# Kernel tuning notes

Hardware: AMD Instinct MI355X
Metric: run time of the kernel (lower is better)

Reference implementation:

```python
import jax, jax.numpy as jnp
import numpy as np

NC = 16       # class_nums
C = 128       # in_channel == EMBEND_DIM
NS = 8192     # support points
NQ = 30000    # query points
EPS = 1e-8


def setup_inputs() -> dict:
    key = jax.random.key(0)
    ks = jax.random.split(key, 7)
    support_features = jax.random.normal(ks[0], (NS, C), dtype=jnp.float32)
    support_labels = jax.random.randint(ks[1], (NS,), 0, NC)
    query_features = jax.random.normal(ks[2], (NQ, C), dtype=jnp.float32)
    # proj = Linear(2C+1 -> C) + ReLU + Linear(C -> 128)
    s1 = 1.0 / np.sqrt(2 * C + 1)
    W1 = jax.random.uniform(ks[3], (2 * C + 1, C), minval=-s1, maxval=s1, dtype=jnp.float32)
    b1 = jax.random.uniform(ks[4], (C,), minval=-s1, maxval=s1, dtype=jnp.float32)
    s2 = 1.0 / np.sqrt(C)
    W2 = jax.random.uniform(ks[5], (C, C), minval=-s2, maxval=s2, dtype=jnp.float32)
    b2 = jax.random.uniform(ks[6], (C,), minval=-s2, maxval=s2, dtype=jnp.float32)
    return {"support_features": support_features, "support_labels": support_labels,
            "query_features": query_features, "W1": W1, "b1": b1, "W2": W2, "b2": b2}


def _prototypes(support_features, support_labels):
    # fused scatter-mean replacing the per-class Python loop
    sums = jax.ops.segment_sum(support_features, support_labels, num_segments=NC)  # [Nc, C]
    counts = jax.ops.segment_sum(jnp.ones((support_features.shape[0],), support_features.dtype),
                                 support_labels, num_segments=NC)                   # [Nc]
    return jnp.where(counts[:, None] > 0, sums / jnp.maximum(counts, 1.0)[:, None], 0.0)


def reference(support_features, support_labels, query_features, W1, b1, W2, b2):
    protos = _prototypes(support_features, support_labels)                # [Nc, C]
    # MD_distance: cosine similarity between each query and each class prototype
    qn = query_features / jnp.maximum(jnp.linalg.norm(query_features, axis=-1, keepdims=True), EPS)
    pn = protos / jnp.maximum(jnp.linalg.norm(protos, axis=-1, keepdims=True), EPS)
    cos = jnp.einsum('qc,nc->qn', qn, pn)                                 # [Nq, Nc]
    # proj(cat([query, proto, cos], -1)) without materializing the [Nq,Nc,2C+1] concat:
    # split W1 rows into query part, proto part, and cos part.
    Wq, Wp, Wc = W1[:C], W1[C:2 * C], W1[2 * C]                           # [C,C],[C,C],[C]
    h = jax.nn.relu(jnp.einsum('qc,ch->qh', query_features, Wq)[:, None, :]
                    + jnp.einsum('nc,ch->nh', protos, Wp)[None, :, :]
                    + cos[:, :, None] * Wc[None, None, :]
                    + b1)                                                 # [Nq, Nc, C]
    similarity = jnp.einsum('qnh,ho->qno', h, W2) + b2                    # [Nq, Nc, 128]
    return similarity, cos[:, :, None]
```

## Files before the change

kernel.cpp:

```cpp
#include <hip/hip_runtime.h>

#define NQ_ 30000
#define NC_ 16
#define C_  128
#define NS_ 8192
#define QB  16
#define NBLK (NQ_/QB)

typedef __attribute__((ext_vector_type(4))) float  f32x4;
typedef __attribute__((ext_vector_type(8))) short  s16x8;

#define WS_PART  0
#define WS_PCNT  65536
#define WS_T     66048
#define WS_PACK  68096

__device__ inline short f2bf(float x){
  unsigned u = __float_as_uint(x);
  u += 0x7fffu + ((u >> 16) & 1u);
  return (short)(u >> 16);
}

__global__ __launch_bounds__(256) void protoA(const float* __restrict__ sf,
                                              const int* __restrict__ lbl,
                                              const float* __restrict__ W1,
                                              const float* __restrict__ W2,
                                              float* __restrict__ ws){
  const int b = blockIdx.x;
  const int t = threadIdx.x;
  if (b < 256){
    __shared__ int ll[512];
    const int cls = b >> 4;
    const int ch  = b & 15;
    const int r0  = ch * 512;
    *(int2*)&ll[t*2] = *(const int2*)&lbl[r0 + t*2];
    __syncthreads();
    const int sub = t >> 7;
    const int c   = t & 127;
    const int i0  = sub * 256;
    float s0 = 0.f, s1 = 0.f; int cnt = 0;
    #pragma unroll 4
    for (int i = 0; i < 256; i += 2){
      if (ll[i0+i]   == cls){ s0 += sf[(size_t)(r0+i0+i  )*C_ + c]; ++cnt; }
      if (ll[i0+i+1] == cls){ s1 += sf[(size_t)(r0+i0+i+1)*C_ + c]; ++cnt; }
    }
    ws[WS_PART + ((size_t)(cls*32 + ch*2 + sub))*C_ + c] = s0 + s1;
    if (c == 0) ws[WS_PCNT + cls*32 + ch*2 + sub] = (float)cnt;
  } else {
    short* packo = (short*)(ws + WS_PACK);
    const int g0 = (b - 256)*2048 + t*8;
    const int gg = g0 & 16383;
    const int ln = (gg >> 3) & 63, ks = (gg >> 9) & 3, wvv = gg >> 11;
    const int kb = ks*32 + ((ln >> 4) & 3)*8;
    const int col = wvv*16 + (ln & 15);
    const float* src = (g0 < 16384) ? W2 : W1;
    s16x8 v;
    #pragma unroll
    for (int i = 0; i < 8; ++i) v[i] = f2bf(src[(size_t)(kb + i)*C_ + col]);
    *(s16x8*)&packo[g0] = v;
  }
}

__global__ __launch_bounds__(128) void protoB(const float* __restrict__ W1,
                                              const float* __restrict__ b1,
                                              float* __restrict__ ws){
  __shared__ float pr[C_];
  __shared__ float rns;
  const int n = blockIdx.x;
  const int h = threadIdx.x;
  float s = 0.f;
  #pragma unroll 8
  for (int ch = 0; ch < 32; ++ch) s += ws[WS_PART + ((size_t)(n*32 + ch))*C_ + h];
  float cnt = 0.f;
  #pragma unroll 8
  for (int ch = 0; ch < 32; ++ch) cnt += ws[WS_PCNT + n*32 + ch];
  const float pv = (cnt > 0.f) ? s / fmaxf(cnt, 1.f) : 0.f;
  pr[h] = pv;
  __syncthreads();
  if (h < 64){
    float q = pr[h]*pr[h] + pr[h+64]*pr[h+64];
    q += __shfl_xor(q, 1);  q += __shfl_xor(q, 2);  q += __shfl_xor(q, 4);
    q += __shfl_xor(q, 8);  q += __shfl_xor(q, 16); q += __shfl_xor(q, 32);
    if (h == 0) rns = 1.f / fmaxf(sqrtf(q), 1e-8f);
  }
  __syncthreads();
  {
    short* packo = (short*)(ws + WS_PACK);
    const int k = h;
    const int gg = ((k >> 5)*64 + ((k >> 3) & 3)*16 + n)*8 + (k & 7);
    packo[32768 + gg] = f2bf(pv * rns);
  }
  float acc = b1[h];
  #pragma unroll 8
  for (int c = 0; c < C_; ++c) acc = fmaf(pr[c], W1[(size_t)(C_ + c)*C_ + h], acc);
  ws[WS_T + n*C_ + h] = acc;
}

__global__ __launch_bounds__(256, 4) void fused_main(const float* __restrict__ qfeat,
                                                     const float* __restrict__ W1,
                                                     const float* __restrict__ b2,
                                                     const float* __restrict__ ws,
                                                     float* __restrict__ out){
  __shared__ __align__(16) char un[16384];
  __shared__ float qw[QB][132];
  __shared__ float tl16[NC_][132];
  __shared__ float cosl[QB][NC_];
  __shared__ float rqn[QB];
  __shared__ float wcl[C_];

  float (*qfs)[132] = (float(*)[132])un;
  short* hfrag = (short*)un;

  const int t    = threadIdx.x;
  const int lane = t & 63;
  const int wv   = t >> 6;
  const int fr   = lane & 15;
  const int fg   = lane >> 4;
  const int qbase = blockIdx.x * QB;
  float* out_cos = out + (size_t)NQ_ * NC_ * C_;
  const short* pack = (const short*)(ws + WS_PACK);

  {
    const int idx = t * 8, q = idx >> 7, c = idx & 127;
    *(f32x4*)&qfs[q][c]      = *(const f32x4*)(qfeat + (size_t)qbase*C_ + idx);
    *(f32x4*)&qfs[q][c+4]    = *(const f32x4*)(qfeat + (size_t)qbase*C_ + idx + 4);
    *(f32x4*)&tl16[q][c]     = *(const f32x4*)(ws + WS_T + idx);
    *(f32x4*)&tl16[q][c+4]   = *(const f32x4*)(ws + WS_T + idx + 4);
    if (t < 32) *(f32x4*)&wcl[t*4] = *(const f32x4*)(W1 + 2*C_*C_ + t*4);
  }
  __syncthreads();

  if (t < 128){
    int q = t >> 3; int c0 = (t & 7) * 16;
    float s = 0.f;
    #pragma unroll
    for (int m = 0; m < 16; ++m){ float v = qfs[q][c0+m]; s = fmaf(v, v, s); }
    s += __shfl_xor(s, 1); s += __shfl_xor(s, 2); s += __shfl_xor(s, 4);
    if ((t & 7) == 0) rqn[q] = 1.f / fmaxf(sqrtf(s), 1e-8f);
  }

  s16x8 qfr[4];
  #pragma unroll
  for (int ks = 0; ks < 4; ++ks){
    const int c0 = ks*32 + fg*8;
    f32x4 a = *(const f32x4*)&qfs[fr][c0];
    f32x4 b = *(const f32x4*)&qfs[fr][c0+4];
    s16x8 v;
    v[0]=f2bf(a[0]); v[1]=f2bf(a[1]); v[2]=f2bf(a[2]); v[3]=f2bf(a[3]);
    v[4]=f2bf(b[0]); v[5]=f2bf(b[1]); v[6]=f2bf(b[2]); v[7]=f2bf(b[3]);
    qfr[ks] = v;
  }
  s16x8 w2f[2][4];
  float b2v[2];
  #pragma unroll
  for (int j = 0; j < 2; ++j){
    const int tt = wv*2 + j;
    #pragma unroll
    for (int ks = 0; ks < 4; ++ks)
      w2f[j][ks] = *(const s16x8*)&pack[((tt*4 + ks)*64 + lane)*8];
    b2v[j] = b2[tt*16 + fr];
  }
  __syncthreads();

  #pragma unroll
  for (int j = 0; j < 2; ++j){
    const int tt = wv*2 + j;
    f32x4 dq = {0.f,0.f,0.f,0.f};
    #pragma unroll
    for (int ks = 0; ks < 4; ++ks)
      dq = __builtin_amdgcn_mfma_f32_16x16x32_bf16(qfr[ks],
             *(const s16x8*)&pack[16384 + ((tt*4 + ks)*64 + lane)*8], dq, 0,0,0);
    #pragma unroll
    for (int r = 0; r < 4; ++r) qw[fg*4 + r][tt*16 + fr] = dq[r];
  }
  if (wv == 0){
    f32x4 dc = {0.f,0.f,0.f,0.f};
    #pragma unroll
    for (int ks = 0; ks < 4; ++ks)
      dc = __builtin_amdgcn_mfma_f32_16x16x32_bf16(qfr[ks],
             *(const s16x8*)&pack[32768 + (ks*64 + lane)*8], dc, 0,0,0);
    #pragma unroll
    for (int r = 0; r < 4; ++r){
      const int q = fg*4 + r;
      const float cv = dc[r] * rqn[q];
      cosl[q][fr] = cv;
      out_cos[(size_t)(qbase + q)*NC_ + fr] = cv;
    }
  }
  __syncthreads();

  const int k0 = wv*32 + fg*8;
  const f32x4 t8a = *(const f32x4*)&tl16[fr][k0];
  const f32x4 t8b = *(const f32x4*)&tl16[fr][k0+4];
  const f32x4 w8a = *(const f32x4*)&wcl[k0];
  const f32x4 w8b = *(const f32x4*)&wcl[k0+4];

  #pragma unroll
  for (int chunk = 0; chunk < 4; ++chunk){
    const int q0 = chunk * 4;
    #pragma unroll
    for (int qq = 0; qq < 4; ++qq){
      const int q = q0 + qq;
      f32x4 qa = *(const f32x4*)&qw[q][k0];
      f32x4 qb = *(const f32x4*)&qw[q][k0+4];
      const float cv = cosl[q][fr];
      s16x8 hv;
      #pragma unroll
      for (int jj = 0; jj < 4; ++jj)
        hv[jj] = f2bf(fmaxf(fmaf(cv, w8a[jj], qa[jj] + t8a[jj]), 0.f));
      #pragma unroll
      for (int jj = 0; jj < 4; ++jj)
        hv[4+jj] = f2bf(fmaxf(fmaf(cv, w8b[jj], qb[jj] + t8b[jj]), 0.f));
      *(s16x8*)&hfrag[qq*2048 + wv*512 + lane*8] = hv;
    }
    __syncthreads();
    #pragma unroll
    for (int qq = 0; qq < 4; ++qq){
      const short* hb = &hfrag[qq*2048 + lane*8];
      s16x8 a0 = *(const s16x8*)&hb[0];
      s16x8 a1 = *(const s16x8*)&hb[512];
      s16x8 a2 = *(const s16x8*)&hb[1024];
      s16x8 a3 = *(const s16x8*)&hb[1536];
      const size_t qout = (size_t)(qbase + q0 + qq) * (NC_*C_);
      #pragma unroll
      for (int j = 0; j < 2; ++j){
        f32x4 acc = {b2v[j], b2v[j], b2v[j], b2v[j]};
        acc = __builtin_amdgcn_mfma_f32_16x16x32_bf16(a0, w2f[j][0], acc, 0,0,0);
        acc = __builtin_amdgcn_mfma_f32_16x16x32_bf16(a1, w2f[j][1], acc, 0,0,0);
        acc = __builtin_amdgcn_mfma_f32_16x16x32_bf16(a2, w2f[j][2], acc, 0,0,0);
        acc = __builtin_amdgcn_mfma_f32_16x16x32_bf16(a3, w2f[j][3], acc, 0,0,0);
        const int ocol = (wv*2 + j)*16 + fr;
        #pragma unroll
        for (int r = 0; r < 4; ++r)
          out[qout + (fg*4 + r)*C_ + ocol] = acc[r];
      }
    }
    __syncthreads();
  }
}

extern "C" void kernel_launch(void* const* d_in, const int* in_sizes, int n_in,
                              void* d_out, int out_size, void* d_ws, size_t ws_size,
                              hipStream_t stream){
  const float* sf  = (const float*)d_in[0];
  const int*   lbl = (const int*)  d_in[1];
  const float* qf  = (const float*)d_in[2];
  const float* W1  = (const float*)d_in[3];
  const float* b1  = (const float*)d_in[4];
  const float* W2  = (const float*)d_in[5];
  const float* b2  = (const float*)d_in[6];
  float* ws  = (float*)d_ws;
  float* out = (float*)d_out;

  protoA<<<272, 256, 0, stream>>>(sf, lbl, W1, W2, ws);
  protoB<<<NC_, 128, 0, stream>>>(W1, b1, ws);
  fused_main<<<NBLK, 256, 0, stream>>>(qf, W1, b2, ws, out);
}
```

Baseline: 82.12 us.

## Process 32 queries per block in fused kernel and split protoB matvec across 512 threads

The fused main kernel now handles 32 queries per block instead of 16. It computes two sets of query MFMA fragments, and two waves compute the cosine tile, so the per-block setup (tl16, W2 fragments, wc, syncs) is amortized over twice as many queries. Bounds checks were added because 30000 is not a multiple of 32. protoB splits the 128-long prototype×W1 matvec across four thread groups, with a shared-memory reduction to shorten its serial chain. The trade-offs are fewer blocks and lower occupancy (launch bounds drop from 4 to 3 blocks) plus more registers per thread.

```diff
diff --git a/kernel.cpp b/kernel.cpp
--- a/kernel.cpp
+++ b/kernel.cpp
@@ -4,8 +4,8 @@
 #define NC_ 16
 #define C_  128
 #define NS_ 8192
-#define QB  16
-#define NBLK (NQ_/QB)
+#define QB2 32
+#define NBLK2 ((NQ_ + QB2 - 1)/QB2)
 
 typedef __attribute__((ext_vector_type(4))) float  f32x4;
 typedef __attribute__((ext_vector_type(8))) short  s16x8;
@@ -61,51 +61,57 @@
   }
 }
 
-__global__ __launch_bounds__(128) void protoB(const float* __restrict__ W1,
+__global__ __launch_bounds__(512) void protoB(const float* __restrict__ W1,
                                               const float* __restrict__ b1,
                                               float* __restrict__ ws){
   __shared__ float pr[C_];
+  __shared__ float sacc[4][C_];
   __shared__ float rns;
   const int n = blockIdx.x;
-  const int h = threadIdx.x;
-  float s = 0.f;
-  #pragma unroll 8
-  for (int ch = 0; ch < 32; ++ch) s += ws[WS_PART + ((size_t)(n*32 + ch))*C_ + h];
-  float cnt = 0.f;
-  #pragma unroll 8
-  for (int ch = 0; ch < 32; ++ch) cnt += ws[WS_PCNT + n*32 + ch];
-  const float pv = (cnt > 0.f) ? s / fmaxf(cnt, 1.f) : 0.f;
-  pr[h] = pv;
-  __syncthreads();
-  if (h < 64){
-    float q = pr[h]*pr[h] + pr[h+64]*pr[h+64];
+  const int t = threadIdx.x;
+  const int h = t & 127;
+  const int part = t >> 7;
+  if (t < 128){
+    float s = 0.f, cnt = 0.f;
+    #pragma unroll 8
+    for (int ch = 0; ch < 32; ++ch) s   += ws[WS_PART + ((size_t)(n*32 + ch))*C_ + h];
+    #pragma unroll 8
+    for (int ch = 0; ch < 32; ++ch) cnt += ws[WS_PCNT + n*32 + ch];
+    pr[h] = (cnt > 0.f) ? s / fmaxf(cnt, 1.f) : 0.f;
+  }
+  __syncthreads();
+  if (t < 64){
+    float q = pr[t]*pr[t] + pr[t+64]*pr[t+64];
     q += __shfl_xor(q, 1);  q += __shfl_xor(q, 2);  q += __shfl_xor(q, 4);
     q += __shfl_xor(q, 8);  q += __shfl_xor(q, 16); q += __shfl_xor(q, 32);
-    if (h == 0) rns = 1.f / fmaxf(sqrtf(q), 1e-8f);
-  }
-  __syncthreads();
+    if (t == 0) rns = 1.f / fmaxf(sqrtf(q), 1e-8f);
+  }
   {
+    float a = 0.f;
+    const int c0 = part * 32;
+    #pragma unroll 8
+    for (int c = c0; c < c0 + 32; ++c) a = fmaf(pr[c], W1[(size_t)(C_ + c)*C_ + h], a);
+    sacc[part][h] = a;
+  }
+  __syncthreads();
+  if (t < 128){
     short* packo = (short*)(ws + WS_PACK);
-    const int k = h;
-    const int gg = ((k >> 5)*64 + ((k >> 3) & 3)*16 + n)*8 + (k & 7);
-    packo[32768 + gg] = f2bf(pv * rns);
-  }
-  float acc = b1[h];
-  #pragma unroll 8
-  for (int c = 0; c < C_; ++c) acc = fmaf(pr[c], W1[(size_t)(C_ + c)*C_ + h], acc);
-  ws[WS_T + n*C_ + h] = acc;
-}
-
-__global__ __launch_bounds__(256, 4) void fused_main(const float* __restrict__ qfeat,
+    const int gg = ((h >> 5)*64 + ((h >> 3) & 3)*16 + n)*8 + (h & 7);
+    packo[32768 + gg] = f2bf(pr[h] * rns);
+    ws[WS_T + n*C_ + h] = b1[h] + ((sacc[0][h] + sacc[1][h]) + (sacc[2][h] + sacc[3][h]));
+  }
+}
+
+__global__ __launch_bounds__(256, 3) void fused_main(const float* __restrict__ qfeat,
                                                      const float* __restrict__ W1,
                                                      const float* __restrict__ b2,
                                                      const float* __restrict__ ws,
                                                      float* __restrict__ out){
-  __shared__ __align__(16) char un[16384];
-  __shared__ float qw[QB][132];
+  __shared__ __align__(16) char un[16896];
+  __shared__ float qw[QB2][132];
   __shared__ float tl16[NC_][132];
-  __shared__ float cosl[QB][NC_];
-  __shared__ float rqn[QB];
+  __shared__ float cosl[QB2][NC_];
+  __shared__ float rqn[QB2];
   __shared__ float wcl[C_];
 
   float (*qfs)[132] = (float(*)[132])un;
@@ -116,22 +122,27 @@
   const int wv   = t >> 6;
   const int fr   = lane & 15;
   const int fg   = lane >> 4;
-  const int qbase = blockIdx.x * QB;
+  const int qbase = blockIdx.x * QB2;
   float* out_cos = out + (size_t)NQ_ * NC_ * C_;
   const short* pack = (const short*)(ws + WS_PACK);
 
   {
-    const int idx = t * 8, q = idx >> 7, c = idx & 127;
-    *(f32x4*)&qfs[q][c]      = *(const f32x4*)(qfeat + (size_t)qbase*C_ + idx);
-    *(f32x4*)&qfs[q][c+4]    = *(const f32x4*)(qfeat + (size_t)qbase*C_ + idx + 4);
-    *(f32x4*)&tl16[q][c]     = *(const f32x4*)(ws + WS_T + idx);
-    *(f32x4*)&tl16[q][c+4]   = *(const f32x4*)(ws + WS_T + idx + 4);
+    const int q = t >> 3, c = (t & 7) * 16;
+    int gr = qbase + q; if (gr > NQ_ - 1) gr = NQ_ - 1;
+    const float* src = qfeat + (size_t)gr*C_ + c;
+    *(f32x4*)&qfs[q][c]    = *(const f32x4*)(src);
+    *(f32x4*)&qfs[q][c+4]  = *(const f32x4*)(src + 4);
+    *(f32x4*)&qfs[q][c+8]  = *(const f32x4*)(src + 8);
+    *(f32x4*)&qfs[q][c+12] = *(const f32x4*)(src + 12);
+    const int r2 = t >> 4, c2 = (t & 15) * 8;
+    *(f32x4*)&tl16[r2][c2]   = *(const f32x4*)(ws + WS_T + r2*C_ + c2);
+    *(f32x4*)&tl16[r2][c2+4] = *(const f32x4*)(ws + WS_T + r2*C_ + c2 + 4);
     if (t < 32) *(f32x4*)&wcl[t*4] = *(const f32x4*)(W1 + 2*C_*C_ + t*4);
   }
   __syncthreads();
 
-  if (t < 128){
-    int q = t >> 3; int c0 = (t & 7) * 16;
+  {
+    const int q = t >> 3, c0 = (t & 7) * 16;
     float s = 0.f;
     #pragma unroll
     for (int m = 0; m < 16; ++m){ float v = qfs[q][c0+m]; s = fmaf(v, v, s); }
@@ -139,7 +150,7 @@
     if ((t & 7) == 0) rqn[q] = 1.f / fmaxf(sqrtf(s), 1e-8f);
   }
 
-  s16x8 qfr[4];
+  s16x8 qfrA[4], qfrB[4];
   #pragma unroll
   for (int ks = 0; ks < 4; ++ks){
     const int c0 = ks*32 + fg*8;
@@ -148,7 +159,13 @@
     s16x8 v;
     v[0]=f2bf(a[0]); v[1]=f2bf(a[1]); v[2]=f2bf(a[2]); v[3]=f2bf(a[3]);
     v[4]=f2bf(b[0]); v[5]=f2bf(b[1]); v[6]=f2bf(b[2]); v[7]=f2bf(b[3]);
-    qfr[ks] = v;
+    qfrA[ks] = v;
+    f32x4 a2 = *(const f32x4*)&qfs[fr+16][c0];
+    f32x4 b2x = *(const f32x4*)&qfs[fr+16][c0+4];
+    s16x8 w;
+    w[0]=f2bf(a2[0]); w[1]=f2bf(a2[1]); w[2]=f2bf(a2[2]); w[3]=f2bf(a2[3]);
+    w[4]=f2bf(b2x[0]); w[5]=f2bf(b2x[1]); w[6]=f2bf(b2x[2]); w[7]=f2bf(b2x[3]);
+    qfrB[ks] = w;
   }
   s16x8 w2f[2][4];
   float b2v[2];
@@ -163,28 +180,32 @@
   __syncthreads();
 
   #pragma unroll
-  for (int j = 0; j < 2; ++j){
-    const int tt = wv*2 + j;
-    f32x4 dq = {0.f,0.f,0.f,0.f};
+  for (int g = 0; g < 2; ++g){
+    #pragma unroll
+    for (int j = 0; j < 2; ++j){
+      const int tt = wv*2 + j;
+      f32x4 dq = {0.f,0.f,0.f,0.f};
+      #pragma unroll
+      for (int ks = 0; ks < 4; ++ks)
+        dq = __builtin_amdgcn_mfma_f32_16x16x32_bf16(g ? qfrB[ks] : qfrA[ks],
+               *(const s16x8*)&pack[16384 + ((tt*4 + ks)*64 + lane)*8], dq, 0,0,0);
+      #pragma unroll
+      for (int r = 0; r < 4; ++r) qw[g*16 + fg*4 + r][tt*16 + fr] = dq[r];
+    }
+  }
+  if (wv < 2){
+    f32x4 dc = {0.f,0.f,0.f,0.f};
     #pragma unroll
     for (int ks = 0; ks < 4; ++ks)
-      dq = __builtin_amdgcn_mfma_f32_16x16x32_bf16(qfr[ks],
-             *(const s16x8*)&pack[16384 + ((tt*4 + ks)*64 + lane)*8], dq, 0,0,0);
-    #pragma unroll
-    for (int r = 0; r < 4; ++r) qw[fg*4 + r][tt*16 + fr] = dq[r];
-  }
-  if (wv == 0){
-    f32x4 dc = {0.f,0.f,0.f,0.f};
-    #pragma unroll
-    for (int ks = 0; ks < 4; ++ks)
-      dc = __builtin_amdgcn_mfma_f32_16x16x32_bf16(qfr[ks],
+      dc = __builtin_amdgcn_mfma_f32_16x16x32_bf16(wv ? qfrB[ks] : qfrA[ks],
              *(const s16x8*)&pack[32768 + (ks*64 + lane)*8], dc, 0,0,0);
     #pragma unroll
     for (int r = 0; r < 4; ++r){
-      const int q = fg*4 + r;
+      const int q = wv*16 + fg*4 + r;
       const float cv = dc[r] * rqn[q];
       cosl[q][fr] = cv;
-      out_cos[(size_t)(qbase + q)*NC_ + fr] = cv;
+      if (qbase + q < NQ_)
+        out_cos[(size_t)(qbase + q)*NC_ + fr] = cv;
     }
   }
   __syncthreads();
@@ -196,8 +217,9 @@
   const f32x4 w8b = *(const f32x4*)&wcl[k0+4];
 
   #pragma unroll
-  for (int chunk = 0; chunk < 4; ++chunk){
+  for (int chunk = 0; chunk < 8; ++chunk){
     const int q0 = chunk * 4;
+    if (qbase + q0 >= NQ_) break;
     #pragma unroll
     for (int qq = 0; qq < 4; ++qq){
       const int q = q0 + qq;
@@ -253,6 +275,6 @@
   float* out = (float*)d_out;
 
   protoA<<<272, 256, 0, stream>>>(sf, lbl, W1, W2, ws);
-  protoB<<<NC_, 128, 0, stream>>>(W1, b1, ws);
-  fused_main<<<NBLK, 256, 0, stream>>>(qf, W1, b2, ws, out);
-}
+  protoB<<<NC_, 512, 0, stream>>>(W1, b1, ws);
+  fused_main<<<NBLK2, 256, 0, stream>>>(qf, W1, b2, ws, out);
+}
```

New measurement: 75.08 us. 8.6% less time.
